# Kernel optimization log

Hardware: AMD Instinct MI355X
Metric: run time of the kernel (lower is better)

Reference implementation:

```python
import jax, jax.numpy as jnp
import numpy as np

V, E, H = 32000, 32, 128
B, T = 2, 512


def setup_inputs() -> dict:
    key = jax.random.key(0)
    ks = jax.random.split(key, 12)
    s = lambda k, shape, scale=0.05: jax.random.normal(k, shape, dtype=jnp.float32) * scale
    return {
        "x": jax.random.randint(ks[0], (B, T), 0, V, dtype=jnp.int64),
        "hidden": jnp.zeros((1, B, H), dtype=jnp.float32),
        "embed_table": s(ks[1], (V, E)),
        "W_ih": s(ks[2], (H, E)),
        "W_hh": s(ks[3], (H, H)),
        "b_ih": jnp.zeros((H,), jnp.float32),
        "b_hh": jnp.zeros((H,), jnp.float32),
        "W1": s(ks[4], (H, H)),
        "W2": s(ks[5], (H, H)),
        "v": s(ks[6], (H,)),
        "Wp": s(ks[7], (H, 2 * H)),
        "bp": jnp.zeros((H,), jnp.float32),
        "Wfc": s(ks[8], (V, H)),
        "bfc": jnp.zeros((V,), jnp.float32),
    }


def reference(x, hidden, embed_table, W_ih, W_hh, b_ih, b_hh, W1, W2, v, Wp, bp, Wfc, bfc):
    # Embedding: (B, T, E)
    emb = embed_table[x]

    # Single-layer tanh RNN (batch_first). Precompute input projections.
    xp = jnp.einsum('bte,he->bth', emb, W_ih) + b_ih + b_hh  # (B,T,H)

    def step(h, x_t):  # h: (B,H), x_t: (B,H)
        h_new = jnp.tanh(x_t + h @ W_hh.T)
        return h_new, h_new

    h0 = hidden[0]  # (B,H)
    h_last, rnn_out = jax.lax.scan(step, h0, jnp.swapaxes(xp, 0, 1))
    rnn_out = jnp.swapaxes(rnn_out, 0, 1)  # (B,T,H)
    hidden_out = h_last[None]  # (1,B,H)

    # Additive (Bahdanau) self-attention with causal mask.
    query = rnn_out @ W1.T  # (B,T,H)
    keys = rnn_out @ W2.T   # (B,T,H)
    # scores: (B,T,T) via (B,T,T,H) broadcast as in the original module
    scores = jnp.einsum('btsh,h->bts', jnp.tanh(query[:, :, None, :] + keys[:, None, :, :]), v)
    causal = jnp.triu(jnp.ones((T, T), bool), k=1)  # mask future s > t
    scores = jnp.where(causal[None], -jnp.inf, scores)
    weights = jax.nn.softmax(scores, axis=-1)
    weights = jnp.nan_to_num(weights)
    context = jnp.einsum('bts,bsh->bth', weights, rnn_out)

    combined = jnp.concatenate([rnn_out, context], axis=-1)  # (B,T,2H)
    out = jax.nn.relu(combined @ Wp.T + bp)  # dropout is identity in eval
    logits = out @ Wfc.T + bfc  # (B,T,V)
    return logits, hidden_out, weights
```

## Files before the change

kernel.cpp:

```cpp
#include <hip/hip_runtime.h>
#include <hip/hip_bf16.h>

#define T 512
#define H 128
#define V 32000
#define B 2

typedef __attribute__((ext_vector_type(8))) short bf16x8;
typedef __attribute__((ext_vector_type(4))) float f32x4;

__device__ __forceinline__ unsigned short f2bf(float f){
  unsigned int u = __float_as_uint(f);
  u = (u + 0x7FFFu + ((u >> 16) & 1u)) >> 16;
  return (unsigned short)u;
}

__device__ __forceinline__ float fast_tanh(float x){
  x = fminf(8.f, fmaxf(-8.f, x));
  float e = __expf(2.f * x);
  return (e - 1.f) / (e + 1.f);
}

__global__ __launch_bounds__(128) void embed_kernel(const int* __restrict__ x,
    const float* __restrict__ table, const float* __restrict__ W_ih,
    const float* __restrict__ b_ih, const float* __restrict__ b_hh,
    float* __restrict__ xp){
  int bt = blockIdx.x;
  int i = threadIdx.x;
  __shared__ __align__(16) float e[32];
  if (i < 32) e[i] = table[(size_t)x[bt] * 32 + i];
  __syncthreads();
  const float* wr = W_ih + i * 32;
  float a0 = 0.f, a1 = 0.f, a2 = 0.f, a3 = 0.f;
  #pragma unroll
  for (int k = 0; k < 32; k += 4){
    float4 w4 = *(const float4*)(wr + k);
    float4 e4 = *(const float4*)(e + k);
    a0 += w4.x * e4.x; a1 += w4.y * e4.y; a2 += w4.z * e4.z; a3 += w4.w * e4.w;
  }
  xp[(size_t)bt * H + i] = (a0 + a1) + (a2 + a3) + b_ih[i] + b_hh[i];
}

__global__ __launch_bounds__(256) void rnn_kernel(const float* __restrict__ xp,
    const float* __restrict__ hidden, const float* __restrict__ W_hh,
    float* __restrict__ rnn, float* __restrict__ hid_out){
  int b = blockIdx.x;
  int tid = threadIdx.x;
  int i = tid >> 1, half = tid & 1;
  float w[64];
  const float* wrow = W_hh + (size_t)i * H + half * 64;
  #pragma unroll
  for (int j = 0; j < 64; ++j) w[j] = wrow[j];
  __shared__ __align__(16) float hb[2][H];
  if (half == 0) hb[0][i] = hidden[b * H + i];
  __syncthreads();
  const float* xpp = xp + (size_t)b * T * H + i;
  float xv = xpp[0];
  float hn = 0.f;
  int cur = 0;
  for (int step = 0; step < T; ++step){
    float xn = (step < T - 1) ? xpp[(size_t)(step + 1) * H] : 0.f;
    const float* hs = hb[cur] + half * 64;
    float a0 = 0.f, a1 = 0.f, a2 = 0.f, a3 = 0.f;
    #pragma unroll
    for (int j = 0; j < 16; ++j){
      float4 hv = *(const float4*)(hs + j * 4);
      a0 += hv.x * w[4*j];   a1 += hv.y * w[4*j+1];
      a2 += hv.z * w[4*j+2]; a3 += hv.w * w[4*j+3];
    }
    float sum = (a0 + a1) + (a2 + a3);
    sum += __shfl_xor(sum, 1);
    hn = fast_tanh(xv + sum);
    if (half == 0){
      hb[cur ^ 1][i] = hn;
      rnn[(size_t)b * T * H + (size_t)step * H + i] = hn;
    }
    __syncthreads();
    xv = xn;
    cur ^= 1;
  }
  if (half == 0) hid_out[b * H + i] = hn;
}

__global__ __launch_bounds__(256) void qk_kernel(const float* __restrict__ rnn,
    const float* __restrict__ W1, const float* __restrict__ W2,
    float* __restrict__ q, float* __restrict__ ky){
  int bt = blockIdx.x;
  int tid = threadIdx.x;
  __shared__ __align__(16) float r[H];
  if (tid < H) r[tid] = rnn[(size_t)bt * H + tid];
  __syncthreads();
  int i = tid & (H - 1);
  const float* wrow = ((tid < H) ? W1 : W2) + (size_t)i * H;
  float a0 = 0.f, a1 = 0.f, a2 = 0.f, a3 = 0.f;
  #pragma unroll 8
  for (int k = 0; k < H; k += 4){
    float4 w4 = *(const float4*)(wrow + k);
    float4 r4 = *(const float4*)(r + k);
    a0 += w4.x * r4.x; a1 += w4.y * r4.y; a2 += w4.z * r4.z; a3 += w4.w * r4.w;
  }
  float res = (a0 + a1) + (a2 + a3);
  if (tid < H) q[(size_t)bt * H + i] = res;
  else         ky[(size_t)bt * H + i] = res;
}

__global__ __launch_bounds__(256) void attn_kernel(const float* __restrict__ rnn,
    const float* __restrict__ q, const float* __restrict__ ky,
    const float* __restrict__ v, const float* __restrict__ Wp,
    const float* __restrict__ bp, float* __restrict__ wout,
    unsigned short* __restrict__ outb){
  int bt = blockIdx.x;
  int b = bt >> 9, t = bt & (T - 1);
  int tid = threadIdx.x;
  __shared__ __align__(16) float qL[H], vL[H], rrL[H], ctxL[H];
  __shared__ __align__(16) float scL[T], wL[T];
  __shared__ float red[4], red2[4];
  if (tid < H){
    qL[tid]  = q[(size_t)bt * H + tid];
    vL[tid]  = v[tid];
    rrL[tid] = rnn[(size_t)bt * H + tid];
  }
  __syncthreads();
  for (int s = tid; s < T; s += 256){
    float sc = -1e30f;
    if (s <= t){
      const float* kr = ky + (size_t)(b * T + s) * H;
      float a0 = 0.f, a1 = 0.f, a2 = 0.f, a3 = 0.f;
      #pragma unroll 4
      for (int h = 0; h < H; h += 4){
        float4 kv = *(const float4*)(kr + h);
        float4 qv = *(const float4*)(qL + h);
        float4 vv = *(const float4*)(vL + h);
        a0 += fast_tanh(qv.x + kv.x) * vv.x;
        a1 += fast_tanh(qv.y + kv.y) * vv.y;
        a2 += fast_tanh(qv.z + kv.z) * vv.z;
        a3 += fast_tanh(qv.w + kv.w) * vv.w;
      }
      sc = (a0 + a1) + (a2 + a3);
    }
    scL[s] = sc;
  }
  __syncthreads();
  float m = -1e30f;
  for (int s = tid; s < T; s += 256) m = fmaxf(m, scL[s]);
  #pragma unroll
  for (int o = 32; o > 0; o >>= 1) m = fmaxf(m, __shfl_xor(m, o));
  if ((tid & 63) == 0) red[tid >> 6] = m;
  __syncthreads();
  float mx = fmaxf(fmaxf(red[0], red[1]), fmaxf(red[2], red[3]));
  float ls = 0.f;
  for (int s = tid; s < T; s += 256){
    float e = (s <= t) ? __expf(scL[s] - mx) : 0.f;
    wL[s] = e; ls += e;
  }
  #pragma unroll
  for (int o = 32; o > 0; o >>= 1) ls += __shfl_xor(ls, o);
  if ((tid & 63) == 0) red2[tid >> 6] = ls;
  __syncthreads();
  float inv = 1.f / (red2[0] + red2[1] + red2[2] + red2[3]);
  for (int s = tid; s < T; s += 256){
    float wv = wL[s] * inv;
    wL[s] = wv;
    wout[(size_t)bt * T + s] = wv;
  }
  __syncthreads();
  if (tid < H){
    const float* rb = rnn + (size_t)b * T * H + tid;
    float c0 = 0.f, c1 = 0.f, c2 = 0.f, c3 = 0.f;
    int s = 0;
    for (; s + 3 <= t; s += 4){
      c0 += wL[s]     * rb[(size_t)s * H];
      c1 += wL[s + 1] * rb[(size_t)(s + 1) * H];
      c2 += wL[s + 2] * rb[(size_t)(s + 2) * H];
      c3 += wL[s + 3] * rb[(size_t)(s + 3) * H];
    }
    for (; s <= t; ++s) c0 += wL[s] * rb[(size_t)s * H];
    ctxL[tid] = (c0 + c1) + (c2 + c3);
  }
  __syncthreads();
  if (tid < H){
    const float* wp = Wp + (size_t)tid * (2 * H);
    float a0 = 0.f, a1 = 0.f, a2 = 0.f, a3 = 0.f;
    #pragma unroll 8
    for (int k = 0; k < H; k += 4){
      float4 w4 = *(const float4*)(wp + k);
      float4 r4 = *(const float4*)(rrL + k);
      a0 += w4.x * r4.x; a1 += w4.y * r4.y; a2 += w4.z * r4.z; a3 += w4.w * r4.w;
    }
    #pragma unroll 8
    for (int k = 0; k < H; k += 4){
      float4 w4 = *(const float4*)(wp + H + k);
      float4 c4 = *(const float4*)(ctxL + k);
      a0 += w4.x * c4.x; a1 += w4.y * c4.y; a2 += w4.z * c4.z; a3 += w4.w * c4.w;
    }
    float o = bp[tid] + (a0 + a1) + (a2 + a3);
    o = fmaxf(o, 0.f);
    outb[(size_t)bt * H + tid] = f2bf(o);
  }
}

__global__ __launch_bounds__(256) void cvt_kernel(const float* __restrict__ src,
    unsigned short* __restrict__ dst){
  size_t idx = ((size_t)blockIdx.x * 256 + threadIdx.x) * 4;
  float4 f = *(const float4*)(src + idx);
  ushort4 o;
  o.x = f2bf(f.x); o.y = f2bf(f.y); o.z = f2bf(f.z); o.w = f2bf(f.w);
  *(ushort4*)(dst + idx) = o;
}

__global__ __launch_bounds__(256) void gemm_kernel(const unsigned short* __restrict__ Ab,
    const unsigned short* __restrict__ Bb, const float* __restrict__ bfc,
    float* __restrict__ Cout){
  __shared__ __align__(16) unsigned short As[64 * 136];
  __shared__ __align__(16) unsigned short Bs[128 * 136];
  int tid = threadIdx.x;
  int nBase = blockIdx.x * 128;
  int mBase = blockIdx.y * 64;
  #pragma unroll
  for (int it = 0; it < 4; ++it){
    int idx = tid + it * 256;
    int row = idx >> 4, kc = (idx & 15) * 8;
    uint4 d = *(const uint4*)(Ab + (size_t)(mBase + row) * H + kc);
    *(uint4*)(As + row * 136 + kc) = d;
  }
  #pragma unroll
  for (int it = 0; it < 8; ++it){
    int idx = tid + it * 256;
    int row = idx >> 4, kc = (idx & 15) * 8;
    uint4 d = *(const uint4*)(Bb + (size_t)(nBase + row) * H + kc);
    *(uint4*)(Bs + row * 136 + kc) = d;
  }
  __syncthreads();
  int l = tid & 63, wv = tid >> 6;
  f32x4 acc[8];
  #pragma unroll
  for (int i = 0; i < 8; ++i) acc[i] = (f32x4){0.f, 0.f, 0.f, 0.f};
  const unsigned short* Ap = As + (wv * 16 + (l & 15)) * 136 + (l >> 4) * 8;
  const unsigned short* Bp = Bs + (l & 15) * 136 + (l >> 4) * 8;
  #pragma unroll
  for (int k0 = 0; k0 < 128; k0 += 32){
    bf16x8 af = *(const bf16x8*)(Ap + k0);
    #pragma unroll
    for (int sub = 0; sub < 8; ++sub){
      bf16x8 bfr = *(const bf16x8*)(Bp + sub * 16 * 136 + k0);
      acc[sub] = __builtin_amdgcn_mfma_f32_16x16x32_bf16(af, bfr, acc[sub], 0, 0, 0);
    }
  }
  int row0 = mBase + wv * 16 + (l >> 4) * 4;
  int col0 = nBase + (l & 15);
  #pragma unroll
  for (int sub = 0; sub < 8; ++sub){
    int c = col0 + sub * 16;
    float bias = bfc[c];
    #pragma unroll
    for (int r = 0; r < 4; ++r){
      Cout[(size_t)(row0 + r) * V + c] = acc[sub][r] + bias;
    }
  }
}

extern "C" void kernel_launch(void* const* d_in, const int* in_sizes, int n_in,
                              void* d_out, int out_size, void* d_ws, size_t ws_size,
                              hipStream_t stream){
  const int*   x      = (const int*)d_in[0];
  const float* hidden = (const float*)d_in[1];
  const float* table  = (const float*)d_in[2];
  const float* W_ih   = (const float*)d_in[3];
  const float* W_hh   = (const float*)d_in[4];
  const float* b_ih   = (const float*)d_in[5];
  const float* b_hh   = (const float*)d_in[6];
  const float* W1     = (const float*)d_in[7];
  const float* W2     = (const float*)d_in[8];
  const float* v      = (const float*)d_in[9];
  const float* Wp     = (const float*)d_in[10];
  const float* bp     = (const float*)d_in[11];
  const float* Wfc    = (const float*)d_in[12];
  const float* bfc    = (const float*)d_in[13];

  float* out     = (float*)d_out;
  float* logits  = out;
  float* hid_out = out + (size_t)B * T * V;
  float* w_out   = hid_out + (size_t)B * H;

  float* xp  = (float*)d_ws;
  float* rnn = xp  + (size_t)B * T * H;
  float* q   = rnn + (size_t)B * T * H;
  float* ky  = q   + (size_t)B * T * H;
  unsigned short* outb = (unsigned short*)(ky + (size_t)B * T * H);
  unsigned short* wfcb = outb + (size_t)B * T * H;

  embed_kernel<<<B * T, 128, 0, stream>>>(x, table, W_ih, b_ih, b_hh, xp);
  rnn_kernel<<<B, 256, 0, stream>>>(xp, hidden, W_hh, rnn, hid_out);
  qk_kernel<<<B * T, 256, 0, stream>>>(rnn, W1, W2, q, ky);
  attn_kernel<<<B * T, 256, 0, stream>>>(rnn, q, ky, v, Wp, bp, w_out, outb);
  cvt_kernel<<<(V * H) / 1024, 256, 0, stream>>>(Wfc, wfcb);
  gemm_kernel<<<dim3(V / 128, (B * T) / 64), 256, 0, stream>>>(outb, wfcb, bfc, logits);
}
```

Before: 513.3 us.

## Fuse Wfc conversion into embed kernel and keep GEMM B tile in registers

Merges the Wfc fp32-to-bf16 conversion into the embedding prep kernel as extra blocks, so one launch is removed and the conversion runs off the critical path ahead of the serial RNN. The logits GEMM now launches one block per 128-column slice, holds that slice of Wfc in registers, and loops over all 16 M-blocks, reading A straight from global memory with no LDS staging or syncs. This reuses B across M but cuts the grid to 250 blocks and raises register pressure (launch_bounds 256,1). The RNN weight load is also vectorized to float4.

```diff
diff --git a/kernel.cpp b/kernel.cpp
--- a/kernel.cpp
+++ b/kernel.cpp
@@ -21,27 +21,39 @@
   return (e - 1.f) / (e + 1.f);
 }
 
-__global__ __launch_bounds__(128) void embed_kernel(const int* __restrict__ x,
+__global__ __launch_bounds__(128) void prep_kernel(const int* __restrict__ x,
     const float* __restrict__ table, const float* __restrict__ W_ih,
     const float* __restrict__ b_ih, const float* __restrict__ b_hh,
-    float* __restrict__ xp){
-  int bt = blockIdx.x;
-  int i = threadIdx.x;
+    const float* __restrict__ Wfc,
+    float* __restrict__ xp, unsigned short* __restrict__ wfcb){
+  int blk = blockIdx.x;
+  int tid = threadIdx.x;
   __shared__ __align__(16) float e[32];
-  if (i < 32) e[i] = table[(size_t)x[bt] * 32 + i];
-  __syncthreads();
-  const float* wr = W_ih + i * 32;
-  float a0 = 0.f, a1 = 0.f, a2 = 0.f, a3 = 0.f;
-  #pragma unroll
-  for (int k = 0; k < 32; k += 4){
-    float4 w4 = *(const float4*)(wr + k);
-    float4 e4 = *(const float4*)(e + k);
-    a0 += w4.x * e4.x; a1 += w4.y * e4.y; a2 += w4.z * e4.z; a3 += w4.w * e4.w;
-  }
-  xp[(size_t)bt * H + i] = (a0 + a1) + (a2 + a3) + b_ih[i] + b_hh[i];
-}
-
-__global__ __launch_bounds__(256) void rnn_kernel(const float* __restrict__ xp,
+  if (blk < B * T){
+    if (tid < 32) e[tid] = table[(size_t)x[blk] * 32 + tid];
+    __syncthreads();
+    const float* wr = W_ih + tid * 32;
+    float a0 = 0.f, a1 = 0.f, a2 = 0.f, a3 = 0.f;
+    #pragma unroll
+    for (int k = 0; k < 32; k += 4){
+      float4 w4 = *(const float4*)(wr + k);
+      float4 e4 = *(const float4*)(e + k);
+      a0 += w4.x * e4.x; a1 += w4.y * e4.y; a2 += w4.z * e4.z; a3 += w4.w * e4.w;
+    }
+    xp[(size_t)blk * H + tid] = (a0 + a1) + (a2 + a3) + b_ih[tid] + b_hh[tid];
+  } else {
+    size_t base = (size_t)(blk - B * T) * 1024 + (size_t)tid * 8;
+    float4 f0 = *(const float4*)(Wfc + base);
+    float4 f1 = *(const float4*)(Wfc + base + 4);
+    ushort4 o0, o1;
+    o0.x = f2bf(f0.x); o0.y = f2bf(f0.y); o0.z = f2bf(f0.z); o0.w = f2bf(f0.w);
+    o1.x = f2bf(f1.x); o1.y = f2bf(f1.y); o1.z = f2bf(f1.z); o1.w = f2bf(f1.w);
+    *(ushort4*)(wfcb + base) = o0;
+    *(ushort4*)(wfcb + base + 4) = o1;
+  }
+}
+
+__global__ __launch_bounds__(256, 1) void rnn_kernel(const float* __restrict__ xp,
     const float* __restrict__ hidden, const float* __restrict__ W_hh,
     float* __restrict__ rnn, float* __restrict__ hid_out){
   int b = blockIdx.x;
@@ -50,7 +62,10 @@
   float w[64];
   const float* wrow = W_hh + (size_t)i * H + half * 64;
   #pragma unroll
-  for (int j = 0; j < 64; ++j) w[j] = wrow[j];
+  for (int j = 0; j < 64; j += 4){
+    float4 t4 = *(const float4*)(wrow + j);
+    w[j] = t4.x; w[j+1] = t4.y; w[j+2] = t4.z; w[j+3] = t4.w;
+  }
   __shared__ __align__(16) float hb[2][H];
   if (half == 0) hb[0][i] = hidden[b * H + i];
   __syncthreads();
@@ -199,62 +214,45 @@
   }
 }
 
-__global__ __launch_bounds__(256) void cvt_kernel(const float* __restrict__ src,
-    unsigned short* __restrict__ dst){
-  size_t idx = ((size_t)blockIdx.x * 256 + threadIdx.x) * 4;
-  float4 f = *(const float4*)(src + idx);
-  ushort4 o;
-  o.x = f2bf(f.x); o.y = f2bf(f.y); o.z = f2bf(f.z); o.w = f2bf(f.w);
-  *(ushort4*)(dst + idx) = o;
-}
-
-__global__ __launch_bounds__(256) void gemm_kernel(const unsigned short* __restrict__ Ab,
+__global__ __launch_bounds__(256, 1) void gemm_kernel(const unsigned short* __restrict__ Ab,
     const unsigned short* __restrict__ Bb, const float* __restrict__ bfc,
     float* __restrict__ Cout){
-  __shared__ __align__(16) unsigned short As[64 * 136];
-  __shared__ __align__(16) unsigned short Bs[128 * 136];
-  int tid = threadIdx.x;
+  int tid = threadIdx.x;
+  int l = tid & 63, wv = tid >> 6;
+  int lm = l & 15, lq = l >> 4;
   int nBase = blockIdx.x * 128;
-  int mBase = blockIdx.y * 64;
-  #pragma unroll
-  for (int it = 0; it < 4; ++it){
-    int idx = tid + it * 256;
-    int row = idx >> 4, kc = (idx & 15) * 8;
-    uint4 d = *(const uint4*)(Ab + (size_t)(mBase + row) * H + kc);
-    *(uint4*)(As + row * 136 + kc) = d;
-  }
-  #pragma unroll
-  for (int it = 0; it < 8; ++it){
-    int idx = tid + it * 256;
-    int row = idx >> 4, kc = (idx & 15) * 8;
-    uint4 d = *(const uint4*)(Bb + (size_t)(nBase + row) * H + kc);
-    *(uint4*)(Bs + row * 136 + kc) = d;
-  }
-  __syncthreads();
-  int l = tid & 63, wv = tid >> 6;
-  f32x4 acc[8];
-  #pragma unroll
-  for (int i = 0; i < 8; ++i) acc[i] = (f32x4){0.f, 0.f, 0.f, 0.f};
-  const unsigned short* Ap = As + (wv * 16 + (l & 15)) * 136 + (l >> 4) * 8;
-  const unsigned short* Bp = Bs + (l & 15) * 136 + (l >> 4) * 8;
-  #pragma unroll
-  for (int k0 = 0; k0 < 128; k0 += 32){
-    bf16x8 af = *(const bf16x8*)(Ap + k0);
+  bf16x8 bw[32];
+  const unsigned short* bp = Bb + (size_t)(nBase + lm) * H + lq * 8;
+  #pragma unroll
+  for (int sub = 0; sub < 8; ++sub)
+    #pragma unroll
+    for (int kk = 0; kk < 4; ++kk)
+      bw[sub * 4 + kk] = *(const bf16x8*)(bp + (size_t)sub * 16 * H + kk * 32);
+  float bias[8];
+  #pragma unroll
+  for (int sub = 0; sub < 8; ++sub) bias[sub] = bfc[nBase + lm + sub * 16];
+  #pragma unroll 1
+  for (int mb = 0; mb < 16; ++mb){
+    int rowA = mb * 64 + wv * 16 + lm;
+    const unsigned short* ap = Ab + (size_t)rowA * H + lq * 8;
+    bf16x8 af[4];
+    #pragma unroll
+    for (int kk = 0; kk < 4; ++kk) af[kk] = *(const bf16x8*)(ap + kk * 32);
+    f32x4 acc[8];
+    #pragma unroll
+    for (int s = 0; s < 8; ++s) acc[s] = (f32x4){0.f, 0.f, 0.f, 0.f};
+    #pragma unroll
+    for (int kk = 0; kk < 4; ++kk)
+      #pragma unroll
+      for (int sub = 0; sub < 8; ++sub)
+        acc[sub] = __builtin_amdgcn_mfma_f32_16x16x32_bf16(af[kk], bw[sub * 4 + kk], acc[sub], 0, 0, 0);
+    int row0 = mb * 64 + wv * 16 + lq * 4;
     #pragma unroll
     for (int sub = 0; sub < 8; ++sub){
-      bf16x8 bfr = *(const bf16x8*)(Bp + sub * 16 * 136 + k0);
-      acc[sub] = __builtin_amdgcn_mfma_f32_16x16x32_bf16(af, bfr, acc[sub], 0, 0, 0);
-    }
-  }
-  int row0 = mBase + wv * 16 + (l >> 4) * 4;
-  int col0 = nBase + (l & 15);
-  #pragma unroll
-  for (int sub = 0; sub < 8; ++sub){
-    int c = col0 + sub * 16;
-    float bias = bfc[c];
-    #pragma unroll
-    for (int r = 0; r < 4; ++r){
-      Cout[(size_t)(row0 + r) * V + c] = acc[sub][r] + bias;
+      int c = nBase + lm + sub * 16;
+      #pragma unroll
+      for (int r = 0; r < 4; ++r)
+        Cout[(size_t)(row0 + r) * V + c] = acc[sub][r] + bias[sub];
     }
   }
 }
@@ -289,10 +287,9 @@
   unsigned short* outb = (unsigned short*)(ky + (size_t)B * T * H);
   unsigned short* wfcb = outb + (size_t)B * T * H;
 
-  embed_kernel<<<B * T, 128, 0, stream>>>(x, table, W_ih, b_ih, b_hh, xp);
+  prep_kernel<<<B * T + (V * H) / 1024, 128, 0, stream>>>(x, table, W_ih, b_ih, b_hh, Wfc, xp, wfcb);
   rnn_kernel<<<B, 256, 0, stream>>>(xp, hidden, W_hh, rnn, hid_out);
   qk_kernel<<<B * T, 256, 0, stream>>>(rnn, W1, W2, q, ky);
   attn_kernel<<<B * T, 256, 0, stream>>>(rnn, q, ky, v, Wp, bp, w_out, outb);
-  cvt_kernel<<<(V * H) / 1024, 256, 0, stream>>>(Wfc, wfcb);
-  gemm_kernel<<<dim3(V / 128, (B * T) / 64), 256, 0, stream>>>(outb, wfcb, bfc, logits);
-}
+  gemm_kernel<<<V / 128, 256, 0, stream>>>(outb, wfcb, bfc, logits);
+}
```

After: 494.5 us. 1.04x faster.
